# Performance work log

Hardware: AMD Instinct MI355X
Metric: run time of the kernel (lower is better)

Reference implementation:

```python
import jax, jax.numpy as jnp
import numpy as np

ALPHA = 0.2          # LeakyReLU negative slope
NEG_INF = -9e15      # mask value from the torch code
B, N, F, E, H, S, T, L = 32, 128, 78, 12, 256, 20, 13, 3


def setup_inputs() -> dict:
    key = jax.random.key(0)
    ks = jax.random.split(key, 20)
    sc = 0.05  # param scale
    inp = {
        "node_features": jax.random.normal(ks[0], (B, N, F), jnp.float32),
        "edge_features": jax.random.normal(ks[1], (B, N, N, E), jnp.float32),
        "adj_matrix": jax.random.randint(ks[2], (B, N, N), 0, 2).astype(jnp.int32),
        "scaffold_features": jax.random.normal(ks[3], (B, S), jnp.float32),
        # node projection (Linear F->H, with bias)
        "W_node": jax.random.normal(ks[4], (F, H), jnp.float32) * sc,
        "b_node": jnp.zeros((H,), jnp.float32),
        # stacked GAT layer params: W (H->H, no bias), a (2H->1, no bias)
        "gat_W": jax.random.normal(ks[5], (L, H, H), jnp.float32) * sc,
        "gat_a": jax.random.normal(ks[6], (L, 2 * H), jnp.float32) * sc,
        # scaffold projection (S->H)
        "W_sc": jax.random.normal(ks[7], (S, H), jnp.float32) * sc,
        "b_sc": jnp.zeros((H,), jnp.float32),
        # graph_pooling MLP: H -> H/2 -> H/4 (shared for graph + scaffold paths)
        "gp_w1": jax.random.normal(ks[8], (H, H // 2), jnp.float32) * sc,
        "gp_b1": jnp.zeros((H // 2,), jnp.float32),
        "gp_w2": jax.random.normal(ks[9], (H // 2, H // 4), jnp.float32) * sc,
        "gp_b2": jnp.zeros((H // 4,), jnp.float32),
        # output MLP: (H/4 + H/4) -> H/2 -> T
        "out_w1": jax.random.normal(ks[10], (H // 2, H // 2), jnp.float32) * sc,
        "out_b1": jnp.zeros((H // 2,), jnp.float32),
        "out_w2": jax.random.normal(ks[11], (H // 2, T), jnp.float32) * sc,
        "out_b2": jnp.zeros((T,), jnp.float32),
    }
    return inp


def _gat_stack(x, adj_matrix, gat_W, gat_a):
    # x: (B,N,H); adj: (B,N,N) int
    mask = adj_matrix > 0
    n_layers, _, h_dim = gat_W.shape
    for l in range(n_layers):
        h = jnp.einsum("bnf,fh->bnh", x, gat_W[l])      # (B,N,H)
        a1, a2 = gat_a[l, :h_dim], gat_a[l, h_dim:]
        # a . [h_i ; h_j] == h_i.a1 + h_j.a2 (exact decomposition of the
        # O(N^2, 2H) concat in the torch code)
        s1 = h @ a1                                       # (B,N)
        s2 = h @ a2                                       # (B,N)
        e = jax.nn.leaky_relu(s1[:, :, None] + s2[:, None, :], ALPHA)
        att = jnp.where(mask, e, NEG_INF)                 # (B,N,N)
        att = jax.nn.softmax(att, axis=-1)
        h_prime = jnp.einsum("bij,bjh->bih", att, h)
        x = jax.nn.relu(h_prime)                          # relu after layer (dropout = identity, eval)
    return x


def _pool(z, gp_w1, gp_b1, gp_w2, gp_b2):
    z = jax.nn.relu(z @ gp_w1 + gp_b1)
    return jax.nn.relu(z @ gp_w2 + gp_b2)


def reference(node_features, edge_features, adj_matrix, scaffold_features,
              W_node, b_node, gat_W, gat_a, W_sc, b_sc,
              gp_w1, gp_b1, gp_w2, gp_b2, out_w1, out_b1, out_w2, out_b2):
    # edge_features is accepted but unused in the original forward
    x = node_features @ W_node + b_node                  # (B,N,H)
    x = _gat_stack(x, adj_matrix, gat_W, gat_a)
    graph = x.mean(axis=1)                               # (B,H)
    g = _pool(graph, gp_w1, gp_b1, gp_w2, gp_b2)         # (B,H/4)
    s = _pool(scaffold_features @ W_sc + b_sc, gp_w1, gp_b1, gp_w2, gp_b2)
    c = jnp.concatenate([g, s], axis=-1)                 # (B,H/2)
    hdn = jax.nn.relu(c @ out_w1 + out_b1)
    return hdn @ out_w2 + out_b2                         # (B,T)
```

## Files before the change

### kernel.cpp

```cpp
#include <hip/hip_runtime.h>
#include <hip/hip_bf16.h>

#define NEG_INF -9.0e15f

using u16 = unsigned short;

__device__ __forceinline__ float b2f(__hip_bfloat16 v) { return __bfloat162float(v); }
__device__ __forceinline__ float ldv(const float* p, int i) { return p[i]; }
__device__ __forceinline__ float ldv(const __hip_bfloat16* p, int i) { return __bfloat162float(p[i]); }

__device__ __forceinline__ void async16(const void* g, void* l) {
    __builtin_amdgcn_global_load_lds(
        (__attribute__((address_space(1))) void*)(g),
        (__attribute__((address_space(3))) void*)(l), 16, 0, 0);
}

__device__ __forceinline__ int sniff(const void* wnode) {
    const u16* w = (const u16*)wnode;
    int lane = threadIdx.x & 63;
    u16 u = w[2 * lane];
    int e = (u >> 7) & 0xFF;
    unsigned long long m = __ballot(e >= 100 && e <= 140);
    return __popcll(m) >= 48;
}


template <int IS_BF>
__device__ __forceinline__ void gat_core(
    char* smem, int t, int row0, int pb0,
    const void* __restrict__ gat_W, const void* __restrict__ gat_a, int l,
    float* __restrict__ hw, float* __restrict__ s1w, float* __restrict__ s2w) {
    float* xsT = (float*)smem;
    const int tx = t & 63, w = t >> 6;
    const int c0 = 4 * tx;
    float acc0[4], acc1[4];
    #pragma unroll
    for (int j = 0; j < 4; ++j) { acc0[j] = 0.f; acc1[j] = 0.f; }

    if (IS_BF) {
        u16* Wb0 = (u16*)(smem + 10240);
        const u16* Wl = (const u16*)gat_W + (size_t)l * 65536;
        auto stage_rows = [&](int r0, int nr, int buf) {
            const char* g = (const char*)Wl + (size_t)r0 * 512;
            char* lp = (char*)(Wb0 + buf * 8192);
            int bytes = nr * 512;
            for (int off = t * 16; off < bytes; off += 4096)
                async16(g + off, lp + off);
        };
        int pb = pb0;
        for (int tt = 0; tt < 8; ++tt) {
            if (tt < 7) stage_rows(32 * (tt + 1), 32, pb ^ 1);
            const u16* Wp = Wb0 + pb * 8192;
            const int k0 = 32 * tt;
            #pragma unroll 8
            for (int kk = 0; kk < 32; ++kk) {
                uint2 wv = *(const uint2*)(Wp + kk * 256 + c0);
                float w0 = __uint_as_float(wv.x << 16);
                float w1 = __uint_as_float(wv.x & 0xffff0000u);
                float w2 = __uint_as_float(wv.y << 16);
                float w3 = __uint_as_float(wv.y & 0xffff0000u);
                float2 xp = *(const float2*)&xsT[(k0 + kk) * 10 + 2 * w];
                acc0[0] += xp.x * w0; acc0[1] += xp.x * w1;
                acc0[2] += xp.x * w2; acc0[3] += xp.x * w3;
                acc1[0] += xp.y * w0; acc1[1] += xp.y * w1;
                acc1[2] += xp.y * w2; acc1[3] += xp.y * w3;
            }
            __syncthreads();
            pb ^= 1;
        }
        const __hip_bfloat16* ga = (const __hip_bfloat16*)gat_a + (size_t)l * 512;
        float d10 = 0.f, d20 = 0.f, d11 = 0.f, d21 = 0.f;
        #pragma unroll
        for (int j = 0; j < 4; ++j) {
            float a1v = b2f(ga[c0 + j]), a2v = b2f(ga[256 + c0 + j]);
            d10 += acc0[j] * a1v; d20 += acc0[j] * a2v;
            d11 += acc1[j] * a1v; d21 += acc1[j] * a2v;
        }
        #pragma unroll
        for (int off = 1; off < 64; off <<= 1) {
            d10 += __shfl_xor(d10, off, 64); d20 += __shfl_xor(d20, off, 64);
            d11 += __shfl_xor(d11, off, 64); d21 += __shfl_xor(d21, off, 64);
        }
        if (tx == 0) {
            s1w[row0 + 2 * w] = d10;     s2w[row0 + 2 * w] = d20;
            s1w[row0 + 2 * w + 1] = d11; s2w[row0 + 2 * w + 1] = d21;
        }
        *(float4*)&hw[(size_t)(row0 + 2 * w) * 256 + c0]     = (float4){acc0[0], acc0[1], acc0[2], acc0[3]};
        *(float4*)&hw[(size_t)(row0 + 2 * w + 1) * 256 + c0] = (float4){acc1[0], acc1[1], acc1[2], acc1[3]};
    } else {
        const float* Wlf = (const float*)gat_W + (size_t)l * 65536;
        const float* gaf = (const float*)gat_a + (size_t)l * 512;
        #pragma unroll 4
        for (int k = 0; k < 256; ++k) {
            float4 wf = *(const float4*)(Wlf + k * 256 + c0);
            float2 xp = *(const float2*)&xsT[k * 10 + 2 * w];
            acc0[0] += xp.x * wf.x; acc0[1] += xp.x * wf.y;
            acc0[2] += xp.x * wf.z; acc0[3] += xp.x * wf.w;
            acc1[0] += xp.y * wf.x; acc1[1] += xp.y * wf.y;
            acc1[2] += xp.y * wf.z; acc1[3] += xp.y * wf.w;
        }
        float d10 = 0.f, d20 = 0.f, d11 = 0.f, d21 = 0.f;
        #pragma unroll
        for (int j = 0; j < 4; ++j) {
            float a1v = gaf[c0 + j], a2v = gaf[256 + c0 + j];
            d10 += acc0[j] * a1v; d20 += acc0[j] * a2v;
            d11 += acc1[j] * a1v; d21 += acc1[j] * a2v;
        }
        #pragma unroll
        for (int off = 1; off < 64; off <<= 1) {
            d10 += __shfl_xor(d10, off, 64); d20 += __shfl_xor(d20, off, 64);
            d11 += __shfl_xor(d11, off, 64); d21 += __shfl_xor(d21, off, 64);
        }
        if (tx == 0) {
            s1w[row0 + 2 * w] = d10;     s2w[row0 + 2 * w] = d20;
            s1w[row0 + 2 * w + 1] = d11; s2w[row0 + 2 * w + 1] = d21;
        }
        *(float4*)&hw[(size_t)(row0 + 2 * w) * 256 + c0]     = (float4){acc0[0], acc0[1], acc0[2], acc0[3]};
        *(float4*)&hw[(size_t)(row0 + 2 * w + 1) * 256 + c0] = (float4){acc1[0], acc1[1], acc1[2], acc1[3]};
    }
}

__device__ __forceinline__ void attn_compute(
    char* smem, int t, int b, int s,
    const float* __restrict__ hw, const float* __restrict__ s1w,
    const float* __restrict__ s2w, const int* __restrict__ adj,
    float ac0[4], float ac1[4]) {
    float (*att_t)[10] = (float (*)[10])smem;
    float* hbuf = (float*)(smem + 5120);
    const int i0 = s << 3;
    const int w = t >> 6, lane = t & 63;
    const char* hbytes = (const char*)(hw + (size_t)b * 32768);
    const int ph = s & 3;
    {
        char* lb = (char*)hbuf;
        const char* g = hbytes + ph * 32768;
        #pragma unroll
        for (int i = 0; i < 8; ++i)
            async16(g + i * 4096 + t * 16, lb + i * 4096 + t * 16);
    }
    {
        int cc0 = lane, cc1 = lane + 64;
        int ir0 = i0 + 2 * w, ir1 = ir0 + 1;
        const int* a0 = adj + (size_t)(b * 128 + ir0) * 128;
        const int* a1 = adj + (size_t)(b * 128 + ir1) * 128;
        int m00 = a0[cc0], m01 = a0[cc1], m10 = a1[cc0], m11 = a1[cc1];
        float sv0 = s1w[b * 128 + ir0], sv1 = s1w[b * 128 + ir1];
        float t0 = s2w[b * 128 + cc0],  t1 = s2w[b * 128 + cc1];
        float e00 = sv0 + t0; e00 = (e00 >= 0.f) ? e00 : 0.2f * e00;
        float e01 = sv0 + t1; e01 = (e01 >= 0.f) ? e01 : 0.2f * e01;
        float e10 = sv1 + t0; e10 = (e10 >= 0.f) ? e10 : 0.2f * e10;
        float e11 = sv1 + t1; e11 = (e11 >= 0.f) ? e11 : 0.2f * e11;
        float v00 = (m00 > 0) ? e00 : NEG_INF;
        float v01 = (m01 > 0) ? e01 : NEG_INF;
        float v10 = (m10 > 0) ? e10 : NEG_INF;
        float v11 = (m11 > 0) ? e11 : NEG_INF;
        float mx0 = fmaxf(v00, v01), mx1 = fmaxf(v10, v11);
        #pragma unroll
        for (int off = 1; off < 64; off <<= 1) {
            mx0 = fmaxf(mx0, __shfl_xor(mx0, off, 64));
            mx1 = fmaxf(mx1, __shfl_xor(mx1, off, 64));
        }
        float p00 = __expf(v00 - mx0), p01 = __expf(v01 - mx0);
        float p10 = __expf(v10 - mx1), p11 = __expf(v11 - mx1);
        float sm0 = p00 + p01, sm1 = p10 + p11;
        #pragma unroll
        for (int off = 1; off < 64; off <<= 1) {
            sm0 += __shfl_xor(sm0, off, 64);
            sm1 += __shfl_xor(sm1, off, 64);
        }
        float inv0 = 1.0f / sm0, inv1 = 1.0f / sm1;
        att_t[cc0][2 * w]     = p00 * inv0;
        att_t[cc1][2 * w]     = p01 * inv0;
        att_t[cc0][2 * w + 1] = p10 * inv1;
        att_t[cc1][2 * w + 1] = p11 * inv1;
    }
    __syncthreads();
    int tx = t & 63, ty = t >> 6;
    #pragma unroll
    for (int j = 0; j < 4; ++j) { ac0[j] = 0.f; ac1[j] = 0.f; }
    for (int c = 0; c < 4; ++c) {
        if (c < 3) {
            char* lb = (char*)hbuf + ((c + 1) & 1) * 32768;
            const char* g = hbytes + (((c + 1 + ph) & 3) * 32768);
            #pragma unroll
            for (int i = 0; i < 8; ++i)
                async16(g + i * 4096 + t * 16, lb + i * 4096 + t * 16);
        }
        const float* hc = hbuf + (c & 1) * 8192;
        const int jb = ((c + ph) & 3) * 32;
        #pragma unroll 4
        for (int jj = 0; jj < 32; ++jj) {
            float4 hv = *(const float4*)&hc[jj * 256 + 4 * tx];
            float2 ap = *(const float2*)&att_t[jb + jj][2 * ty];
            ac0[0] += ap.x * hv.x; ac0[1] += ap.x * hv.y;
            ac0[2] += ap.x * hv.z; ac0[3] += ap.x * hv.w;
            ac1[0] += ap.y * hv.x; ac1[1] += ap.y * hv.y;
            ac1[2] += ap.y * hv.z; ac1[3] += ap.y * hv.w;
        }
        __syncthreads();
    }
}

__global__ __launch_bounds__(256) void k_gat_first(
    const void* __restrict__ nf, const void* __restrict__ Wn_raw,
    const void* __restrict__ bn,
    const void* __restrict__ gat_W, const void* __restrict__ gat_a,
    float* __restrict__ hw, float* __restrict__ s1w, float* __restrict__ s2w) {
    __shared__ __align__(16) char smem[43008];
    const int t = threadIdx.x;
    const int blk = blockIdx.x;
    const int b = blk & 31, s = blk >> 5;
    const int row0 = b * 128 + s * 8;
    const int tx = t & 63, w = t >> 6;
    const int c0 = 4 * tx;
    float* xsT = (float*)smem;
    float acc0[4], acc1[4];

    if (sniff(Wn_raw)) {
        u16* Wb0 = (u16*)(smem + 10240);
        const u16* Wl = (const u16*)gat_W;
        auto stage = [&](const u16* src, int r0, int nr, int buf) {
            const char* g = (const char*)src + (size_t)r0 * 512;
            char* lp = (char*)(Wb0 + buf * 8192);
            int bytes = nr * 512;
            for (int off = t * 16; off < bytes; off += 4096)
                async16(g + off, lp + off);
        };
        auto tile = [&](int buf, int k0, int nr) {
            const u16* Wp = Wb0 + buf * 8192;
            #pragma unroll 8
            for (int kk = 0; kk < nr; ++kk) {
                uint2 wv = *(const uint2*)(Wp + kk * 256 + c0);
                float w0 = __uint_as_float(wv.x << 16);
                float w1 = __uint_as_float(wv.x & 0xffff0000u);
                float w2 = __uint_as_float(wv.y << 16);
                float w3 = __uint_as_float(wv.y & 0xffff0000u);
                float2 xp = *(const float2*)&xsT[(k0 + kk) * 10 + 2 * w];
                acc0[0] += xp.x * w0; acc0[1] += xp.x * w1;
                acc0[2] += xp.x * w2; acc0[3] += xp.x * w3;
                acc1[0] += xp.y * w0; acc1[1] += xp.y * w1;
                acc1[2] += xp.y * w2; acc1[3] += xp.y * w3;
            }
        };
        const u16* Wnl = (const u16*)Wn_raw;
        stage(Wnl, 0, 32, 0);
        const u16* nfu = (const u16*)nf;
        for (int i = t; i < 624; i += 256) {
            int r = i / 78, k = i - r * 78;
            xsT[k * 10 + r] = __uint_as_float(((unsigned)nfu[(row0 + r) * 78 + k]) << 16);
        }
        const __hip_bfloat16* bnb = (const __hip_bfloat16*)bn;
        #pragma unroll
        for (int j = 0; j < 4; ++j) { acc0[j] = b2f(bnb[c0 + j]); acc1[j] = acc0[j]; }
        __syncthreads();
        stage(Wnl, 32, 32, 1);
        tile(0, 0, 32);
        __syncthreads();
        stage(Wnl, 64, 14, 0);
        tile(1, 32, 32);
        __syncthreads();
        stage(Wl, 0, 32, 1);
        tile(0, 64, 14);
        __syncthreads();
        #pragma unroll
        for (int j = 0; j < 4; ++j) {
            xsT[(c0 + j) * 10 + 2 * w]     = acc0[j];
            xsT[(c0 + j) * 10 + 2 * w + 1] = acc1[j];
        }
        __syncthreads();
        gat_core<1>(smem, t, row0, 1, gat_W, gat_a, 0, hw, s1w, s2w);
    } else {
        const float* nff = (const float*)nf;
        for (int i = t; i < 624; i += 256) {
            int r = i / 78, k = i - r * 78;
            xsT[k * 10 + r] = nff[(row0 + r) * 78 + k];
        }
        __syncthreads();
        const float* Wnf = (const float*)Wn_raw;
        const float* bnf = (const float*)bn;
        #pragma unroll
        for (int j = 0; j < 4; ++j) { acc0[j] = bnf[c0 + j]; acc1[j] = acc0[j]; }
        for (int k = 0; k < 78; ++k) {
            float4 wf = *(const float4*)(Wnf + k * 256 + c0);
            float2 xp = *(const float2*)&xsT[k * 10 + 2 * w];
            acc0[0] += xp.x * wf.x; acc0[1] += xp.x * wf.y;
            acc0[2] += xp.x * wf.z; acc0[3] += xp.x * wf.w;
            acc1[0] += xp.y * wf.x; acc1[1] += xp.y * wf.y;
            acc1[2] += xp.y * wf.z; acc1[3] += xp.y * wf.w;
        }
        __syncthreads();
        #pragma unroll
        for (int j = 0; j < 4; ++j) {
            xsT[(c0 + j) * 10 + 2 * w]     = acc0[j];
            xsT[(c0 + j) * 10 + 2 * w + 1] = acc1[j];
        }
        __syncthreads();
        gat_core<0>(smem, t, row0, 0, gat_W, gat_a, 0, hw, s1w, s2w);
    }
}

__global__ __launch_bounds__(256) void k_attn_gat(
    const float* __restrict__ h_in, const float* __restrict__ s1_in,
    const float* __restrict__ s2_in, const int* __restrict__ adj,
    const void* __restrict__ gat_W, const void* __restrict__ gat_a, int l,
    const void* __restrict__ Wn_raw,
    float* __restrict__ h_out, float* __restrict__ s1_out, float* __restrict__ s2_out) {
    __shared__ __align__(16) char smem[74752];
    const int t = threadIdx.x;
    const int blk = blockIdx.x;
    const int b = blk & 31, s = blk >> 5;
    const int row0 = b * 128 + s * 8;
    const int isbf = sniff(Wn_raw);

    float ac0[4], ac1[4];
    attn_compute(smem, t, b, s, h_in, s1_in, s2_in, adj, ac0, ac1);
    const int tx = t & 63, ty = t >> 6;
    const int c0 = 4 * tx;
    float* xsT = (float*)smem;
    if (isbf) {
        u16* Wb0 = (u16*)(smem + 10240);
        const u16* Wl = (const u16*)gat_W + (size_t)l * 65536;
        for (int off = t * 16; off < 16384; off += 4096)
            async16((const char*)Wl + off, (char*)Wb0 + off);
    }
    #pragma unroll
    for (int j = 0; j < 4; ++j) {
        xsT[(c0 + j) * 10 + 2 * ty]     = fmaxf(ac0[j], 0.f);
        xsT[(c0 + j) * 10 + 2 * ty + 1] = fmaxf(ac1[j], 0.f);
    }
    __syncthreads();
    if (isbf)
        gat_core<1>(smem, t, row0, 0, gat_W, gat_a, l, h_out, s1_out, s2_out);
    else
        gat_core<0>(smem, t, row0, 0, gat_W, gat_a, l, h_out, s1_out, s2_out);
}

__global__ __launch_bounds__(256) void k_attn_pool(
    const float* __restrict__ h_in, const float* __restrict__ s1_in,
    const float* __restrict__ s2_in, const int* __restrict__ adj,
    float* __restrict__ gpart) {
    __shared__ __align__(16) char smem[74752];
    const int t = threadIdx.x;
    const int blk = blockIdx.x;
    const int b = blk & 31, s = blk >> 5;
    float ac0[4], ac1[4];
    attn_compute(smem, t, b, s, h_in, s1_in, s2_in, adj, ac0, ac1);
    float (*pool_red)[256] = (float (*)[256])(smem + 70656);
    const int tx = t & 63, ty = t >> 6;
    float4 pr = {(fmaxf(ac0[0],0.f) + fmaxf(ac1[0],0.f)) * (1.f/128.f),
                 (fmaxf(ac0[1],0.f) + fmaxf(ac1[1],0.f)) * (1.f/128.f),
                 (fmaxf(ac0[2],0.f) + fmaxf(ac1[2],0.f)) * (1.f/128.f),
                 (fmaxf(ac0[3],0.f) + fmaxf(ac1[3],0.f)) * (1.f/128.f)};
    *(float4*)&pool_red[ty][4 * tx] = pr;
    __syncthreads();
    if (t < 64) {
        float4 r0 = ((const float4*)&pool_red[0][0])[t];
        float4 r1 = ((const float4*)&pool_red[1][0])[t];
        float4 r2 = ((const float4*)&pool_red[2][0])[t];
        float4 r3 = ((const float4*)&pool_red[3][0])[t];
        float4 o = {r0.x+r1.x+r2.x+r3.x, r0.y+r1.y+r2.y+r3.y,
                    r0.z+r1.z+r2.z+r3.z, r0.w+r1.w+r2.w+r3.w};
        *(float4*)&gpart[((size_t)b * 16 + s) * 256 + 4 * t] = o;
    }
}

template <typename T>
__device__ __forceinline__ void head_body(
    int b, int t, const float* __restrict__ gpart,
    const T* scaf, const T* W_sc, const T* b_sc,
    const T* gp_w1, const T* gp_b1, const T* gp_w2, const T* gp_b2,
    const T* out_w1, const T* out_b1, const T* out_w2, const T* out_b2,
    float* gin_s, float* sproj, float* scaf_s,
    float* red1, float* red2, float* z1g, float* z1s,
    float* cvec, float* hdn, float* outv) {
    float g = 0.f;
    #pragma unroll
    for (int gg = 0; gg < 16; ++gg) g += gpart[((size_t)b * 16 + gg) * 256 + t];
    gin_s[t] = g;
    if (t < 20) scaf_s[t] = ldv(scaf, b * 20 + t);
    __syncthreads();
    {
        float sa = ldv(b_sc, t);
        #pragma unroll
        for (int k = 0; k < 20; ++k) sa += scaf_s[k] * ldv(W_sc, k * 256 + t);
        sproj[t] = sa;
    }
    __syncthreads();
    {
        int j = t & 127, khalf = t >> 7;
        int k0 = khalf * 128;
        float a1 = 0.f, a2 = 0.f;
        #pragma unroll 16
        for (int kk = 0; kk < 128; ++kk) {
            int k = k0 + kk;
            float wv = ldv(gp_w1, k * 128 + j);
            a1 += gin_s[k] * wv;
            a2 += sproj[k] * wv;
        }
        red1[t] = a1; red2[t] = a2;
    }
    __syncthreads();
    if (t < 128) {
        float bb = ldv(gp_b1, t);
        z1g[t] = fmaxf(bb + red1[t] + red1[t + 128], 0.f);
        z1s[t] = fmaxf(bb + red2[t] + red2[t + 128], 0.f);
    }
    __syncthreads();
    {
        int j = t & 63, q = t >> 6;
        int k0 = q * 32;
        float a1 = 0.f, a2 = 0.f;
        #pragma unroll
        for (int kk = 0; kk < 32; ++kk) {
            int k = k0 + kk;
            float wv = ldv(gp_w2, k * 64 + j);
            a1 += z1g[k] * wv;
            a2 += z1s[k] * wv;
        }
        red1[t] = a1; red2[t] = a2;
    }
    __syncthreads();
    if (t < 64) {
        float bb = ldv(gp_b2, t);
        cvec[t]      = fmaxf(bb + red1[t] + red1[t + 64] + red1[t + 128] + red1[t + 192], 0.f);
        cvec[64 + t] = fmaxf(bb + red2[t] + red2[t + 64] + red2[t + 128] + red2[t + 192], 0.f);
    }
    __syncthreads();
    {
        int j = t & 127, khalf = t >> 7;
        int k0 = khalf * 64;
        float a = 0.f;
        #pragma unroll 16
        for (int kk = 0; kk < 64; ++kk) {
            int k = k0 + kk;
            a += cvec[k] * ldv(out_w1, k * 128 + j);
        }
        red1[t] = a;
    }
    __syncthreads();
    if (t < 128) hdn[t] = fmaxf(ldv(out_b1, t) + red1[t] + red1[t + 128], 0.f);
    __syncthreads();
    if (t < 13) {
        float a = ldv(out_b2, t);
        #pragma unroll 16
        for (int k = 0; k < 128; ++k) a += hdn[k] * ldv(out_w2, k * 13 + t);
        outv[t] = a;
    }
}

__global__ __launch_bounds__(256) void k_head(
    const float* __restrict__ gpart, const void* __restrict__ scaf,
    const void* __restrict__ W_sc, const void* __restrict__ b_sc,
    const void* __restrict__ gp_w1, const void* __restrict__ gp_b1,
    const void* __restrict__ gp_w2, const void* __restrict__ gp_b2,
    const void* __restrict__ out_w1, const void* __restrict__ out_b1,
    const void* __restrict__ out_w2, const void* __restrict__ out_b2,
    void* __restrict__ out, const void* __restrict__ Wn) {
    int isbf = sniff(Wn);
    int b = blockIdx.x;
    int t = threadIdx.x;
    __shared__ float gin_s[256], sproj[256], scaf_s[20];
    __shared__ float red1[256], red2[256];
    __shared__ float z1g[128], z1s[128], cvec[128], hdn[128], outv[13];
    if (isbf) {
        head_body<__hip_bfloat16>(b, t, gpart,
            (const __hip_bfloat16*)scaf, (const __hip_bfloat16*)W_sc, (const __hip_bfloat16*)b_sc,
            (const __hip_bfloat16*)gp_w1, (const __hip_bfloat16*)gp_b1,
            (const __hip_bfloat16*)gp_w2, (const __hip_bfloat16*)gp_b2,
            (const __hip_bfloat16*)out_w1, (const __hip_bfloat16*)out_b1,
            (const __hip_bfloat16*)out_w2, (const __hip_bfloat16*)out_b2,
            gin_s, sproj, scaf_s, red1, red2, z1g, z1s, cvec, hdn, outv);
    } else {
        head_body<float>(b, t, gpart,
            (const float*)scaf, (const float*)W_sc, (const float*)b_sc,
            (const float*)gp_w1, (const float*)gp_b1,
            (const float*)gp_w2, (const float*)gp_b2,
            (const float*)out_w1, (const float*)out_b1,
            (const float*)out_w2, (const float*)out_b2,
            gin_s, sproj, scaf_s, red1, red2, z1g, z1s, cvec, hdn, outv);
    }
    __syncthreads();
    if (t < 13) {
        if (isbf) ((__hip_bfloat16*)out)[b * 13 + t] = __float2bfloat16(outv[t]);
        else      ((float*)out)[b * 13 + t] = outv[t];
    }
}

extern "C" void kernel_launch(void* const* d_in, const int* in_sizes, int n_in,
                              void* d_out, int out_size, void* d_ws, size_t ws_size,
                              hipStream_t stream) {
    (void)in_sizes; (void)n_in; (void)out_size; (void)ws_size;
    const void* nf     = d_in[0];
    const int*  adj    = (const int*)d_in[2];
    const void* scaf   = d_in[3];
    const void* W_node = d_in[4];
    const void* b_node = d_in[5];
    const void* gat_W  = d_in[6];
    const void* gat_a  = d_in[7];
    const void* W_sc   = d_in[8];
    const void* b_sc   = d_in[9];
    const void* gp_w1  = d_in[10];
    const void* gp_b1  = d_in[11];
    const void* gp_w2  = d_in[12];
    const void* gp_b2  = d_in[13];
    const void* out_w1 = d_in[14];
    const void* out_b1 = d_in[15];
    const void* out_w2 = d_in[16];
    const void* out_b2 = d_in[17];

    float* ws    = (float*)d_ws;
    float* hA    = ws;
    float* hB    = ws + 1048576;
    float* s1A   = ws + 2097152;
    float* s2A   = ws + 2101248;
    float* s1B   = ws + 2105344;
    float* s2B   = ws + 2109440;
    float* gpart = ws + 2113536;

    k_gat_first<<<512, 256, 0, stream>>>(nf, W_node, b_node, gat_W, gat_a,
                                         hA, s1A, s2A);
    k_attn_gat<<<512, 256, 0, stream>>>(hA, s1A, s2A, adj, gat_W, gat_a, 1,
                                        W_node, hB, s1B, s2B);
    k_attn_gat<<<512, 256, 0, stream>>>(hB, s1B, s2B, adj, gat_W, gat_a, 2,
                                        W_node, hA, s1A, s2A);
    k_attn_pool<<<512, 256, 0, stream>>>(hA, s1A, s2A, adj, gpart);
    k_head<<<32, 256, 0, stream>>>(gpart, scaf, W_sc, b_sc, gp_w1, gp_b1, gp_w2, gp_b2,
                                   out_w1, out_b1, out_w2, out_b2, d_out, W_node);
}
```

Before: 208.0 us.

## Compute attention-weighted aggregation from registers and global loads, dropping LDS staging

Replaces the LDS-staged attention aggregation with a register-only version. Each wave broadcasts its softmax weights via shuffles and reads h rows directly from global memory, rather than async-copying h chunks into double-buffered shared memory and storing attention transposed. This removes the per-chunk block barriers and cuts the shared-memory footprint (74KB down to 43KB or 4KB), which should allow more blocks per CU. The trade-off is that each of the four waves now reads the full 128x256 h tile for its graph from global/L2 separately and adds one shuffle per row.

Result: no change. 210.5 us (+1.2%).

```diff
diff --git a/kernel.cpp b/kernel.cpp
--- a/kernel.cpp
+++ b/kernel.cpp
@@ -120,84 +120,68 @@
     }
 }
 
-__device__ __forceinline__ void attn_compute(
-    char* smem, int t, int b, int s,
+__device__ __forceinline__ void attn_reg(
+    int t, int b, int s,
     const float* __restrict__ hw, const float* __restrict__ s1w,
     const float* __restrict__ s2w, const int* __restrict__ adj,
     float ac0[4], float ac1[4]) {
-    float (*att_t)[10] = (float (*)[10])smem;
-    float* hbuf = (float*)(smem + 5120);
+    const int w = t >> 6, lane = t & 63;
     const int i0 = s << 3;
-    const int w = t >> 6, lane = t & 63;
-    const char* hbytes = (const char*)(hw + (size_t)b * 32768);
-    const int ph = s & 3;
-    {
-        char* lb = (char*)hbuf;
-        const char* g = hbytes + ph * 32768;
-        #pragma unroll
-        for (int i = 0; i < 8; ++i)
-            async16(g + i * 4096 + t * 16, lb + i * 4096 + t * 16);
-    }
-    {
-        int cc0 = lane, cc1 = lane + 64;
-        int ir0 = i0 + 2 * w, ir1 = ir0 + 1;
-        const int* a0 = adj + (size_t)(b * 128 + ir0) * 128;
-        const int* a1 = adj + (size_t)(b * 128 + ir1) * 128;
-        int m00 = a0[cc0], m01 = a0[cc1], m10 = a1[cc0], m11 = a1[cc1];
-        float sv0 = s1w[b * 128 + ir0], sv1 = s1w[b * 128 + ir1];
-        float t0 = s2w[b * 128 + cc0],  t1 = s2w[b * 128 + cc1];
-        float e00 = sv0 + t0; e00 = (e00 >= 0.f) ? e00 : 0.2f * e00;
-        float e01 = sv0 + t1; e01 = (e01 >= 0.f) ? e01 : 0.2f * e01;
-        float e10 = sv1 + t0; e10 = (e10 >= 0.f) ? e10 : 0.2f * e10;
-        float e11 = sv1 + t1; e11 = (e11 >= 0.f) ? e11 : 0.2f * e11;
-        float v00 = (m00 > 0) ? e00 : NEG_INF;
-        float v01 = (m01 > 0) ? e01 : NEG_INF;
-        float v10 = (m10 > 0) ? e10 : NEG_INF;
-        float v11 = (m11 > 0) ? e11 : NEG_INF;
-        float mx0 = fmaxf(v00, v01), mx1 = fmaxf(v10, v11);
-        #pragma unroll
-        for (int off = 1; off < 64; off <<= 1) {
-            mx0 = fmaxf(mx0, __shfl_xor(mx0, off, 64));
-            mx1 = fmaxf(mx1, __shfl_xor(mx1, off, 64));
-        }
-        float p00 = __expf(v00 - mx0), p01 = __expf(v01 - mx0);
-        float p10 = __expf(v10 - mx1), p11 = __expf(v11 - mx1);
-        float sm0 = p00 + p01, sm1 = p10 + p11;
-        #pragma unroll
-        for (int off = 1; off < 64; off <<= 1) {
-            sm0 += __shfl_xor(sm0, off, 64);
-            sm1 += __shfl_xor(sm1, off, 64);
-        }
-        float inv0 = 1.0f / sm0, inv1 = 1.0f / sm1;
-        att_t[cc0][2 * w]     = p00 * inv0;
-        att_t[cc1][2 * w]     = p01 * inv0;
-        att_t[cc0][2 * w + 1] = p10 * inv1;
-        att_t[cc1][2 * w + 1] = p11 * inv1;
-    }
-    __syncthreads();
-    int tx = t & 63, ty = t >> 6;
+    const int ir0 = i0 + 2 * w, ir1 = ir0 + 1;
+    const int* a0 = adj + (size_t)(b * 128 + ir0) * 128;
+    const int* a1 = adj + (size_t)(b * 128 + ir1) * 128;
+    int m00 = a0[lane], m01 = a0[lane + 64], m10 = a1[lane], m11 = a1[lane + 64];
+    float sv0 = s1w[b * 128 + ir0], sv1 = s1w[b * 128 + ir1];
+    float t0 = s2w[b * 128 + lane], t1 = s2w[b * 128 + lane + 64];
+    float e00 = sv0 + t0; e00 = (e00 >= 0.f) ? e00 : 0.2f * e00;
+    float e01 = sv0 + t1; e01 = (e01 >= 0.f) ? e01 : 0.2f * e01;
+    float e10 = sv1 + t0; e10 = (e10 >= 0.f) ? e10 : 0.2f * e10;
+    float e11 = sv1 + t1; e11 = (e11 >= 0.f) ? e11 : 0.2f * e11;
+    float v00 = (m00 > 0) ? e00 : NEG_INF;
+    float v01 = (m01 > 0) ? e01 : NEG_INF;
+    float v10 = (m10 > 0) ? e10 : NEG_INF;
+    float v11 = (m11 > 0) ? e11 : NEG_INF;
+    float mx0 = fmaxf(v00, v01), mx1 = fmaxf(v10, v11);
     #pragma unroll
-    for (int j = 0; j < 4; ++j) { ac0[j] = 0.f; ac1[j] = 0.f; }
-    for (int c = 0; c < 4; ++c) {
-        if (c < 3) {
-            char* lb = (char*)hbuf + ((c + 1) & 1) * 32768;
-            const char* g = hbytes + (((c + 1 + ph) & 3) * 32768);
-            #pragma unroll
-            for (int i = 0; i < 8; ++i)
-                async16(g + i * 4096 + t * 16, lb + i * 4096 + t * 16);
-        }
-        const float* hc = hbuf + (c & 1) * 8192;
-        const int jb = ((c + ph) & 3) * 32;
-        #pragma unroll 4
-        for (int jj = 0; jj < 32; ++jj) {
-            float4 hv = *(const float4*)&hc[jj * 256 + 4 * tx];
-            float2 ap = *(const float2*)&att_t[jb + jj][2 * ty];
-            ac0[0] += ap.x * hv.x; ac0[1] += ap.x * hv.y;
-            ac0[2] += ap.x * hv.z; ac0[3] += ap.x * hv.w;
-            ac1[0] += ap.y * hv.x; ac1[1] += ap.y * hv.y;
-            ac1[2] += ap.y * hv.z; ac1[3] += ap.y * hv.w;
-        }
-        __syncthreads();
+    for (int off = 1; off < 64; off <<= 1) {
+        mx0 = fmaxf(mx0, __shfl_xor(mx0, off, 64));
+        mx1 = fmaxf(mx1, __shfl_xor(mx1, off, 64));
+    }
+    float p00 = __expf(v00 - mx0), p01 = __expf(v01 - mx0);
+    float p10 = __expf(v10 - mx1), p11 = __expf(v11 - mx1);
+    float sm0 = p00 + p01, sm1 = p10 + p11;
+    #pragma unroll
+    for (int off = 1; off < 64; off <<= 1) {
+        sm0 += __shfl_xor(sm0, off, 64);
+        sm1 += __shfl_xor(sm1, off, 64);
+    }
+    float inv0 = 1.0f / sm0, inv1 = 1.0f / sm1;
+    float p00s = p00 * inv0, p01s = p01 * inv0;
+    float p10s = p10 * inv1, p11s = p11 * inv1;
+
+    const float* hb = hw + (size_t)b * 32768;
+    const int c0 = 4 * (t & 63);
+    ac0[0] = 0.f; ac0[1] = 0.f; ac0[2] = 0.f; ac0[3] = 0.f;
+    ac1[0] = 0.f; ac1[1] = 0.f; ac1[2] = 0.f; ac1[3] = 0.f;
+    #pragma unroll 8
+    for (int j = 0; j < 64; ++j) {
+        float a0v = __shfl(p00s, j, 64);
+        float a1v = __shfl(p10s, j, 64);
+        float4 hv = *(const float4*)&hb[(size_t)j * 256 + c0];
+        ac0[0] += a0v * hv.x; ac0[1] += a0v * hv.y;
+        ac0[2] += a0v * hv.z; ac0[3] += a0v * hv.w;
+        ac1[0] += a1v * hv.x; ac1[1] += a1v * hv.y;
+        ac1[2] += a1v * hv.z; ac1[3] += a1v * hv.w;
+    }
+    #pragma unroll 8
+    for (int j = 0; j < 64; ++j) {
+        float a0v = __shfl(p01s, j, 64);
+        float a1v = __shfl(p11s, j, 64);
+        float4 hv = *(const float4*)&hb[(size_t)(j + 64) * 256 + c0];
+        ac0[0] += a0v * hv.x; ac0[1] += a0v * hv.y;
+        ac0[2] += a0v * hv.z; ac0[3] += a0v * hv.w;
+        ac1[0] += a1v * hv.x; ac1[1] += a1v * hv.y;
+        ac1[2] += a1v * hv.z; ac1[3] += a1v * hv.w;
     }
 }
 
@@ -305,7 +289,7 @@
     const void* __restrict__ gat_W, const void* __restrict__ gat_a, int l,
     const void* __restrict__ Wn_raw,
     float* __restrict__ h_out, float* __restrict__ s1_out, float* __restrict__ s2_out) {
-    __shared__ __align__(16) char smem[74752];
+    __shared__ __align__(16) char smem[43008];
     const int t = threadIdx.x;
     const int blk = blockIdx.x;
     const int b = blk & 31, s = blk >> 5;
@@ -313,8 +297,9 @@
     const int isbf = sniff(Wn_raw);
 
     float ac0[4], ac1[4];
-    attn_compute(smem, t, b, s, h_in, s1_in, s2_in, adj, ac0, ac1);
-    const int tx = t & 63, ty = t >> 6;
+    attn_reg(t, b, s, h_in, s1_in, s2_in, adj, ac0, ac1);
+
+    const int tx = t & 63, w = t >> 6;
     const int c0 = 4 * tx;
     float* xsT = (float*)smem;
     if (isbf) {
@@ -325,8 +310,8 @@
     }
     #pragma unroll
     for (int j = 0; j < 4; ++j) {
-        xsT[(c0 + j) * 10 + 2 * ty]     = fmaxf(ac0[j], 0.f);
-        xsT[(c0 + j) * 10 + 2 * ty + 1] = fmaxf(ac1[j], 0.f);
+        xsT[(c0 + j) * 10 + 2 * w]     = fmaxf(ac0[j], 0.f);
+        xsT[(c0 + j) * 10 + 2 * w + 1] = fmaxf(ac1[j], 0.f);
     }
     __syncthreads();
     if (isbf)
@@ -339,13 +324,12 @@
     const float* __restrict__ h_in, const float* __restrict__ s1_in,
     const float* __restrict__ s2_in, const int* __restrict__ adj,
     float* __restrict__ gpart) {
-    __shared__ __align__(16) char smem[74752];
+    __shared__ __align__(16) float pool_red[4][256];
     const int t = threadIdx.x;
     const int blk = blockIdx.x;
     const int b = blk & 31, s = blk >> 5;
     float ac0[4], ac1[4];
-    attn_compute(smem, t, b, s, h_in, s1_in, s2_in, adj, ac0, ac1);
-    float (*pool_red)[256] = (float (*)[256])(smem + 70656);
+    attn_reg(t, b, s, h_in, s1_in, s2_in, adj, ac0, ac1);
     const int tx = t & 63, ty = t >> 6;
     float4 pr = {(fmaxf(ac0[0],0.f) + fmaxf(ac1[0],0.f)) * (1.f/128.f),
                  (fmaxf(ac0[1],0.f) + fmaxf(ac1[1],0.f)) * (1.f/128.f),
```
